# Kernel tuning notes

Measured on AMD Instinct MI355X. Metric: run time of the kernel, lower is better.

## Reference

```python
import jax, jax.numpy as jnp
import numpy as np

B, C_IN, C_OUT, H, K = 256, 64, 64, 1855, 6


def setup_inputs() -> dict:
    key = jax.random.key(0)
    k1, k2, k3, k4 = jax.random.split(key, 4)
    x = jax.random.normal(k1, (B, C_IN, H), dtype=jnp.float32)
    # hex-grid neighbor table; -1 marks missing neighbors (camera boundary).
    neighbors = jax.random.randint(k2, (H, K), 0, H, dtype=jnp.int32)
    # row 0 fully valid is not required -- module uses row 0 to compute total_valid.
    mask = jax.random.uniform(k3, (H, K)) < 0.1
    neighbors = jnp.where(mask, -1, neighbors)
    weight_center = jax.random.normal(k4, (C_OUT, C_IN), dtype=jnp.float32) / np.sqrt(C_IN)
    weight_neighbors = jax.random.normal(jax.random.fold_in(key, 5), (C_OUT, C_IN, K), dtype=jnp.float32) / np.sqrt(C_IN * K)
    bias = jnp.zeros((C_OUT,), dtype=jnp.float32)
    return {"x": x, "neighbors": neighbors, "weight_center": weight_center,
            "weight_neighbors": weight_neighbors, "bias": bias}


def reference(x, neighbors, weight_center, weight_neighbors, bias):
    # x: [B, C_in, H] -> [B, H, C_in]
    xt = jnp.swapaxes(x, 1, 2)
    # center contribution: [B, H, C_out]
    center = jnp.einsum('bhc,oc->bho', xt, weight_center)
    valid = neighbors >= 0                      # [H, K]
    idx = jnp.where(valid, neighbors, 0)        # safe gather indices
    nf = xt[:, idx]                             # [B, H, K, C_in] gathered neighbors
    nf = nf * valid[None, :, :, None].astype(xt.dtype)
    neighbor_contrib = jnp.einsum('bhkc,ock->bho', nf, weight_neighbors)
    # module divides by (#valid neighbors of hexagon 0) + 1
    total_valid = (valid[0].sum() + 1).astype(xt.dtype)
    out = (center + neighbor_contrib) / total_valid + bias
    return jnp.swapaxes(out, 1, 2)              # [B, C_out, H]
```

## Files before the change

### kernel.cpp

```cpp
#include <hip/hip_runtime.h>
#include <hip/hip_bf16.h>

#define B_    256
#define CIN   64
#define COUT  64
#define H_    1855
#define K_    6
#define KDIM  448
#define NSTEP 14
#define HT    64
#define NHT   29

#define HT2   32
#define TPB   58
#define NTILE (TPB * B_)
#define TPBLK 8
#define NBLK  (NTILE / TPBLK)
#define CPX2  (NBLK / 8)

typedef __bf16 bf16x8 __attribute__((ext_vector_type(8)));
typedef float  f32x4  __attribute__((ext_vector_type(4)));

typedef __attribute__((address_space(3))) unsigned int       lds_u32;
typedef const __attribute__((address_space(1))) unsigned int glb_u32;

static __device__ inline unsigned short f2bf(float f) {
    __hip_bfloat16 h = __float2bfloat16(f);
    return *reinterpret_cast<unsigned short*>(&h);
}

__global__ void prep_weights(const float* __restrict__ wc,
                             const float* __restrict__ wn,
                             const int*   __restrict__ nb,
                             unsigned short* __restrict__ W2,
                             float* __restrict__ inv_tv,
                             unsigned short* __restrict__ zbuf) {
    int e = blockIdx.x * 256 + threadIdx.x;
    int j = e & 7;
    int l = (e >> 3) & 63;
    int t = (e >> 9) & 3;
    int s = e >> 11;
    int o = t * 16 + (l & 15);
    int k = s * 32 + (l >> 4) * 8 + j;
    int slot = k >> 6;
    int c = k & 63;
    float v = (slot == 0) ? wc[o * 64 + c]
                          : wn[(o * 64 + c) * 6 + (slot - 1)];
    W2[e] = f2bf(v);
    if (blockIdx.x == 0 && threadIdx.x < 64) zbuf[threadIdx.x] = 0;
    if (e == 0) {
        int cnt = 1;
        #pragma unroll
        for (int q = 0; q < 6; ++q) cnt += (nb[q] >= 0) ? 1 : 0;
        *inv_tv = 1.0f / (float)cnt;
    }
}

__global__ void transpose_bf16(const float* __restrict__ x,
                               unsigned short* __restrict__ xT) {
    __shared__ __align__(16) unsigned short tile[64][72];
    int b  = blockIdx.y;
    int h0 = blockIdx.x * HT;
    int t  = threadIdx.x;
    int ho = t & 63;
    int cq = t >> 6;
    const float* xb = x + (size_t)b * CIN * H_;
    int h = h0 + ho;
    #pragma unroll
    for (int i = 0; i < 16; ++i) {
        int c = i * 4 + cq;
        float v = (h < H_) ? xb[(size_t)c * H_ + h] : 0.f;
        tile[ho][c] = f2bf(v);
    }
    __syncthreads();
    #pragma unroll
    for (int rep = 0; rep < 2; ++rep) {
        int task = rep * 256 + t;
        int hh = task >> 3;
        int j  = task & 7;
        int hw = h0 + hh;
        if (hw < H_) {
            *reinterpret_cast<uint4*>(&xT[((size_t)b * H_ + hw) * 64 + j * 8]) =
                *reinterpret_cast<const uint4*>(&tile[hh][j * 8]);
        }
    }
}

__global__ __launch_bounds__(512, 4) void conv_main(
        const unsigned short* __restrict__ xT,
        const unsigned short* __restrict__ W2,
        const int*   __restrict__ nb,
        const float* __restrict__ bias,
        const float* __restrict__ inv_tv,
        const unsigned short* __restrict__ zbuf,
        float* __restrict__ out) {
    __shared__ __align__(16) unsigned short feat[2][7][HT2][64];

    int bid = blockIdx.x;
    int swz   = (bid & 7) * CPX2 + (bid >> 3);
    int gbase = swz * TPBLK;

    int t = threadIdx.x;
    int w = t >> 6;
    int l = t & 63;

    int lrow = l >> 3;
    int jsrc = (l & 7) ^ lrow;
    int q    = w - 1;

    int og = w & 3, hh = w >> 2;
    int lr = l & 15, lg = l >> 4;
    int hrow = hh * 16 + lr;

    const bf16x8* __restrict__ Wf = reinterpret_cast<const bf16x8*>(W2);
    bf16x8 wr[NSTEP];
    #pragma unroll
    for (int s = 0; s < NSTEP; ++s) wr[s] = Wf[(s * 4 + og) * 64 + l];
    float inv = *inv_tv;
    float bv[4];
    #pragma unroll
    for (int r = 0; r < 4; ++r) bv[r] = bias[og * 16 + lg * 4 + r];

    int nbv[4];
    int bn, h0n;

    if (w < 7) {
        int b0  = gbase / TPB;
        int h00 = (gbase - b0 * TPB) * HT2;
        #pragma unroll
        for (int c = 0; c < 4; ++c) {
            int h = h00 + c * 8 + lrow;
            nbv[c] = (h < H_) ? ((w == 0) ? h : nb[h * 6 + q]) : -1;
        }
        const unsigned short* xb = xT + (size_t)b0 * H_ * 64;
        #pragma unroll
        for (int c = 0; c < 4; ++c) {
            int n = nbv[c];
            const unsigned short* src = (n >= 0)
                ? (xb + (size_t)n * 64 + jsrc * 8) : (zbuf + jsrc * 8);
            __builtin_amdgcn_global_load_lds((glb_u32*)src,
                (lds_u32*)&feat[0][w][c * 8][0], 16, 0, 0);
        }
        int g1 = gbase + 1;
        bn  = g1 / TPB;
        h0n = (g1 - bn * TPB) * HT2;
        #pragma unroll
        for (int c = 0; c < 4; ++c) {
            int h = h0n + c * 8 + lrow;
            nbv[c] = (h < H_) ? ((w == 0) ? h : nb[h * 6 + q]) : -1;
        }
    }

    #pragma unroll 2
    for (int i = 0; i < TPBLK; ++i) {
        if (i < TPBLK - 1 && w < 7) {
            const unsigned short* xb = xT + (size_t)bn * H_ * 64;
            #pragma unroll
            for (int c = 0; c < 4; ++c) {
                int n = nbv[c];
                const unsigned short* src = (n >= 0)
                    ? (xb + (size_t)n * 64 + jsrc * 8) : (zbuf + jsrc * 8);
                __builtin_amdgcn_global_load_lds((glb_u32*)src,
                    (lds_u32*)&feat[(i + 1) & 1][w][c * 8][0], 16, 0, 0);
            }
        }
        if (i < TPBLK - 2 && w < 7) {
            int g2 = gbase + i + 2;
            bn  = g2 / TPB;
            h0n = (g2 - bn * TPB) * HT2;
            #pragma unroll
            for (int c = 0; c < 4; ++c) {
                int h = h0n + c * 8 + lrow;
                nbv[c] = (h < H_) ? ((w == 0) ? h : nb[h * 6 + q]) : -1;
            }
        }
        if (w == 0 || i == TPBLK - 1)
            asm volatile("s_waitcnt vmcnt(4)" ::: "memory");
        else
            asm volatile("s_waitcnt vmcnt(8)" ::: "memory");
        __builtin_amdgcn_s_barrier();
        __builtin_amdgcn_sched_barrier(0);

        int cb = i & 1;
        f32x4 acc = (f32x4){0.f, 0.f, 0.f, 0.f};
        #pragma unroll
        for (int s = 0; s < NSTEP; ++s) {
            int c16 = (((s & 1) * 4 + lg)) ^ (hrow & 7);
            bf16x8 bfrag = *reinterpret_cast<const bf16x8*>(
                    &feat[cb][s >> 1][hrow][c16 * 8]);
            acc = __builtin_amdgcn_mfma_f32_16x16x32_bf16(wr[s], bfrag, acc, 0, 0, 0);
        }

        int g    = gbase + i;
        int curb = g / TPB;
        int curh = (g - curb * TPB) * HT2 + hrow;
        if (curh < H_) {
            float* ob = out + (size_t)curb * COUT * H_ + curh;
            #pragma unroll
            for (int r = 0; r < 4; ++r)
                ob[(size_t)(og * 16 + lg * 4 + r) * H_] = acc[r] * inv + bv[r];
        }

        __builtin_amdgcn_s_barrier();
    }
}

extern "C" void kernel_launch(void* const* d_in, const int* in_sizes, int n_in,
                              void* d_out, int out_size, void* d_ws, size_t ws_size,
                              hipStream_t stream) {
    const float* x    = (const float*)d_in[0];
    const int*   nb   = (const int*)  d_in[1];
    const float* wc   = (const float*)d_in[2];
    const float* wn   = (const float*)d_in[3];
    const float* bias = (const float*)d_in[4];
    float* out = (float*)d_out;

    char* ws = (char*)d_ws;
    unsigned short* W2     = (unsigned short*)ws;
    float*          inv_tv = (float*)(ws + 57344);
    unsigned short* zbuf   = (unsigned short*)(ws + 57472);
    unsigned short* xT     = (unsigned short*)(ws + 57600);

    prep_weights<<<112, 256, 0, stream>>>(wc, wn, nb, W2, inv_tv, zbuf);

    dim3 tgrid(NHT, B_);
    transpose_bf16<<<tgrid, 256, 0, stream>>>(x, xT);
    conv_main<<<NBLK, 512, 0, stream>>>(xT, W2, nb, bias, inv_tv, zbuf, out);
}
```

Baseline: 115.6 us.

## Halve conv block to 4 waves, each computing two output groups

Shrinks the conv block from 8 to 4 wavefronts. Each wave now computes two 16-wide output-channel groups from one shared B fragment, which reuses each LDS read across two MFMAs. The gather work is spread so each wave loads one or two neighbor slots, and the vmcnt waits are adjusted to match. This doubles the per-wave weight registers and gather load count and lowers the thread count per block, trading occupancy and latency hiding for fewer LDS reads.

```diff
diff --git a/kernel.cpp b/kernel.cpp
--- a/kernel.cpp
+++ b/kernel.cpp
@@ -86,7 +86,7 @@
     }
 }
 
-__global__ __launch_bounds__(512, 4) void conv_main(
+__global__ __launch_bounds__(256, 2) void conv_main(
         const unsigned short* __restrict__ xT,
         const unsigned short* __restrict__ W2,
         const int*   __restrict__ nb,
@@ -106,40 +106,61 @@
 
     int lrow = l >> 3;
     int jsrc = (l & 7) ^ lrow;
-    int q    = w - 1;
-
-    int og = w & 3, hh = w >> 2;
+    int slotA = w;
+    int slotB = w + 4;
+    bool hasB = (w < 3);
+    int qA = slotA - 1;
+    int qB = slotB - 1;
+
+    int ogp = w & 1, hh = w >> 1;
     int lr = l & 15, lg = l >> 4;
     int hrow = hh * 16 + lr;
 
     const bf16x8* __restrict__ Wf = reinterpret_cast<const bf16x8*>(W2);
-    bf16x8 wr[NSTEP];
-    #pragma unroll
-    for (int s = 0; s < NSTEP; ++s) wr[s] = Wf[(s * 4 + og) * 64 + l];
+    bf16x8 wr[NSTEP][2];
+    #pragma unroll
+    for (int s = 0; s < NSTEP; ++s)
+        #pragma unroll
+        for (int u = 0; u < 2; ++u)
+            wr[s][u] = Wf[(s * 4 + ogp * 2 + u) * 64 + l];
     float inv = *inv_tv;
-    float bv[4];
-    #pragma unroll
-    for (int r = 0; r < 4; ++r) bv[r] = bias[og * 16 + lg * 4 + r];
-
-    int nbv[4];
+    float bv0[4], bv1[4];
+    #pragma unroll
+    for (int r = 0; r < 4; ++r) {
+        bv0[r] = bias[ogp * 32 + lg * 4 + r];
+        bv1[r] = bias[ogp * 32 + 16 + lg * 4 + r];
+    }
+
+    int nbvA[4], nbvB[4];
     int bn, h0n;
 
-    if (w < 7) {
+    {
         int b0  = gbase / TPB;
         int h00 = (gbase - b0 * TPB) * HT2;
         #pragma unroll
         for (int c = 0; c < 4; ++c) {
             int h = h00 + c * 8 + lrow;
-            nbv[c] = (h < H_) ? ((w == 0) ? h : nb[h * 6 + q]) : -1;
+            nbvA[c] = (h < H_) ? ((qA < 0) ? h : nb[h * 6 + qA]) : -1;
+            nbvB[c] = (hasB && h < H_) ? nb[h * 6 + qB] : -1;
         }
         const unsigned short* xb = xT + (size_t)b0 * H_ * 64;
         #pragma unroll
         for (int c = 0; c < 4; ++c) {
-            int n = nbv[c];
+            int n = nbvA[c];
             const unsigned short* src = (n >= 0)
                 ? (xb + (size_t)n * 64 + jsrc * 8) : (zbuf + jsrc * 8);
             __builtin_amdgcn_global_load_lds((glb_u32*)src,
-                (lds_u32*)&feat[0][w][c * 8][0], 16, 0, 0);
+                (lds_u32*)&feat[0][slotA][c * 8][0], 16, 0, 0);
+        }
+        if (hasB) {
+            #pragma unroll
+            for (int c = 0; c < 4; ++c) {
+                int n = nbvB[c];
+                const unsigned short* src = (n >= 0)
+                    ? (xb + (size_t)n * 64 + jsrc * 8) : (zbuf + jsrc * 8);
+                __builtin_amdgcn_global_load_lds((glb_u32*)src,
+                    (lds_u32*)&feat[0][slotB][c * 8][0], 16, 0, 0);
+            }
         }
         int g1 = gbase + 1;
         bn  = g1 / TPB;
@@ -147,48 +168,63 @@
         #pragma unroll
         for (int c = 0; c < 4; ++c) {
             int h = h0n + c * 8 + lrow;
-            nbv[c] = (h < H_) ? ((w == 0) ? h : nb[h * 6 + q]) : -1;
+            nbvA[c] = (h < H_) ? ((qA < 0) ? h : nb[h * 6 + qA]) : -1;
+            nbvB[c] = (hasB && h < H_) ? nb[h * 6 + qB] : -1;
         }
     }
 
     #pragma unroll 2
     for (int i = 0; i < TPBLK; ++i) {
-        if (i < TPBLK - 1 && w < 7) {
+        if (i < TPBLK - 1) {
             const unsigned short* xb = xT + (size_t)bn * H_ * 64;
+            int nbuf = (i + 1) & 1;
             #pragma unroll
             for (int c = 0; c < 4; ++c) {
-                int n = nbv[c];
+                int n = nbvA[c];
                 const unsigned short* src = (n >= 0)
                     ? (xb + (size_t)n * 64 + jsrc * 8) : (zbuf + jsrc * 8);
                 __builtin_amdgcn_global_load_lds((glb_u32*)src,
-                    (lds_u32*)&feat[(i + 1) & 1][w][c * 8][0], 16, 0, 0);
-            }
-        }
-        if (i < TPBLK - 2 && w < 7) {
+                    (lds_u32*)&feat[nbuf][slotA][c * 8][0], 16, 0, 0);
+            }
+            if (hasB) {
+                #pragma unroll
+                for (int c = 0; c < 4; ++c) {
+                    int n = nbvB[c];
+                    const unsigned short* src = (n >= 0)
+                        ? (xb + (size_t)n * 64 + jsrc * 8) : (zbuf + jsrc * 8);
+                    __builtin_amdgcn_global_load_lds((glb_u32*)src,
+                        (lds_u32*)&feat[nbuf][slotB][c * 8][0], 16, 0, 0);
+                }
+            }
+        }
+        if (i < TPBLK - 2) {
             int g2 = gbase + i + 2;
             bn  = g2 / TPB;
             h0n = (g2 - bn * TPB) * HT2;
             #pragma unroll
             for (int c = 0; c < 4; ++c) {
                 int h = h0n + c * 8 + lrow;
-                nbv[c] = (h < H_) ? ((w == 0) ? h : nb[h * 6 + q]) : -1;
-            }
-        }
-        if (w == 0 || i == TPBLK - 1)
-            asm volatile("s_waitcnt vmcnt(4)" ::: "memory");
+                nbvA[c] = (h < H_) ? ((qA < 0) ? h : nb[h * 6 + qA]) : -1;
+                nbvB[c] = (hasB && h < H_) ? nb[h * 6 + qB] : -1;
+            }
+        }
+        if (w < 3 && i < TPBLK - 1)
+            asm volatile("s_waitcnt vmcnt(16)" ::: "memory");
         else
             asm volatile("s_waitcnt vmcnt(8)" ::: "memory");
         __builtin_amdgcn_s_barrier();
         __builtin_amdgcn_sched_barrier(0);
 
         int cb = i & 1;
-        f32x4 acc = (f32x4){0.f, 0.f, 0.f, 0.f};
+        f32x4 acc0 = (f32x4){0.f, 0.f, 0.f, 0.f};
+        f32x4 acc1 = (f32x4){0.f, 0.f, 0.f, 0.f};
         #pragma unroll
         for (int s = 0; s < NSTEP; ++s) {
             int c16 = (((s & 1) * 4 + lg)) ^ (hrow & 7);
             bf16x8 bfrag = *reinterpret_cast<const bf16x8*>(
                     &feat[cb][s >> 1][hrow][c16 * 8]);
-            acc = __builtin_amdgcn_mfma_f32_16x16x32_bf16(wr[s], bfrag, acc, 0, 0, 0);
+            acc0 = __builtin_amdgcn_mfma_f32_16x16x32_bf16(wr[s][0], bfrag, acc0, 0, 0, 0);
+            acc1 = __builtin_amdgcn_mfma_f32_16x16x32_bf16(wr[s][1], bfrag, acc1, 0, 0, 0);
         }
 
         int g    = gbase + i;
@@ -197,8 +233,10 @@
         if (curh < H_) {
             float* ob = out + (size_t)curb * COUT * H_ + curh;
             #pragma unroll
-            for (int r = 0; r < 4; ++r)
-                ob[(size_t)(og * 16 + lg * 4 + r) * H_] = acc[r] * inv + bv[r];
+            for (int r = 0; r < 4; ++r) {
+                ob[(size_t)(ogp * 32 + lg * 4 + r) * H_]      = acc0[r] * inv + bv0[r];
+                ob[(size_t)(ogp * 32 + 16 + lg * 4 + r) * H_] = acc1[r] * inv + bv1[r];
+            }
         }
 
         __builtin_amdgcn_s_barrier();
@@ -225,5 +263,5 @@
 
     dim3 tgrid(NHT, B_);
     transpose_bf16<<<tgrid, 256, 0, stream>>>(x, xT);
-    conv_main<<<NBLK, 512, 0, stream>>>(xT, W2, nb, bias, inv_tv, zbuf, out);
-}
+    conv_main<<<NBLK, 256, 0, stream>>>(xT, W2, nb, bias, inv_tv, zbuf, out);
+}
```

Result: slower. 119.6 us (+3.5%).

## Load center features directly into registers and spread neighbor gathers over all waves

Applied to the files above, without the earlier changes.

Center-pixel features are now loaded straight from global memory into registers (double-buffered) and fed to MFMA, no longer staged through LDS. The six neighbor slots' gather work is redistributed so all 8 waves issue 3 async global-to-LDS loads each, replacing 7 waves doing 4 each while one wave idled. LDS drops from 7 to 6 slots per buffer and the main loop is fully unrolled. Wait counts are retuned to the new load mix. This risks more register pressure and more VGPR-destination loads in flight.

```diff
diff --git a/kernel.cpp b/kernel.cpp
--- a/kernel.cpp
+++ b/kernel.cpp
@@ -6,7 +6,6 @@
 #define COUT  64
 #define H_    1855
 #define K_    6
-#define KDIM  448
 #define NSTEP 14
 #define HT    64
 #define NHT   29
@@ -94,7 +93,7 @@
         const float* __restrict__ inv_tv,
         const unsigned short* __restrict__ zbuf,
         float* __restrict__ out) {
-    __shared__ __align__(16) unsigned short feat[2][7][HT2][64];
+    __shared__ __align__(16) unsigned short feat[2][6][HT2][64];
 
     int bid = blockIdx.x;
     int swz   = (bid & 7) * CPX2 + (bid >> 3);
@@ -106,89 +105,115 @@
 
     int lrow = l >> 3;
     int jsrc = (l & 7) ^ lrow;
-    int q    = w - 1;
+    int qm[3], rq[3];
+    #pragma unroll
+    for (int c = 0; c < 3; ++c) {
+        int m = w * 3 + c;
+        qm[c] = m >> 2;
+        rq[c] = (m & 3) * 8;
+    }
 
     int og = w & 3, hh = w >> 2;
     int lr = l & 15, lg = l >> 4;
     int hrow = hh * 16 + lr;
+    int sw8  = hrow & 7;
 
     const bf16x8* __restrict__ Wf = reinterpret_cast<const bf16x8*>(W2);
     bf16x8 wr[NSTEP];
     #pragma unroll
     for (int s = 0; s < NSTEP; ++s) wr[s] = Wf[(s * 4 + og) * 64 + l];
+    #pragma unroll
+    for (int s = 0; s < NSTEP; ++s) asm volatile("" : "+v"(wr[s]));
+
     float inv = *inv_tv;
     float bv[4];
     #pragma unroll
     for (int r = 0; r < 4; ++r) bv[r] = bias[og * 16 + lg * 4 + r];
 
-    int nbv[4];
+    int nbv[3];
     int bn, h0n;
-
-    if (w < 7) {
+    bf16x8 cc[2][2];
+
+    {
         int b0  = gbase / TPB;
         int h00 = (gbase - b0 * TPB) * HT2;
         #pragma unroll
-        for (int c = 0; c < 4; ++c) {
-            int h = h00 + c * 8 + lrow;
-            nbv[c] = (h < H_) ? ((w == 0) ? h : nb[h * 6 + q]) : -1;
+        for (int c = 0; c < 3; ++c) {
+            int h = h00 + rq[c] + lrow;
+            nbv[c] = (h < H_) ? nb[h * 6 + qm[c]] : -1;
         }
         const unsigned short* xb = xT + (size_t)b0 * H_ * 64;
         #pragma unroll
-        for (int c = 0; c < 4; ++c) {
+        for (int c = 0; c < 3; ++c) {
             int n = nbv[c];
             const unsigned short* src = (n >= 0)
                 ? (xb + (size_t)n * 64 + jsrc * 8) : (zbuf + jsrc * 8);
             __builtin_amdgcn_global_load_lds((glb_u32*)src,
-                (lds_u32*)&feat[0][w][c * 8][0], 16, 0, 0);
-        }
+                (lds_u32*)&feat[0][qm[c]][rq[c]][0], 16, 0, 0);
+        }
+        int hcl = h00 + hrow; if (hcl >= H_) hcl = H_ - 1;
+        const bf16x8* crow = reinterpret_cast<const bf16x8*>(xb + (size_t)hcl * 64);
+        cc[0][0] = crow[lg];
+        cc[0][1] = crow[4 + lg];
         int g1 = gbase + 1;
         bn  = g1 / TPB;
         h0n = (g1 - bn * TPB) * HT2;
         #pragma unroll
-        for (int c = 0; c < 4; ++c) {
-            int h = h0n + c * 8 + lrow;
-            nbv[c] = (h < H_) ? ((w == 0) ? h : nb[h * 6 + q]) : -1;
-        }
-    }
-
-    #pragma unroll 2
+        for (int c = 0; c < 3; ++c) {
+            int h = h0n + rq[c] + lrow;
+            nbv[c] = (h < H_) ? nb[h * 6 + qm[c]] : -1;
+        }
+    }
+
+    #pragma unroll
     for (int i = 0; i < TPBLK; ++i) {
-        if (i < TPBLK - 1 && w < 7) {
+        if (i < TPBLK - 1) {
             const unsigned short* xb = xT + (size_t)bn * H_ * 64;
+            int nbuf = (i + 1) & 1;
             #pragma unroll
-            for (int c = 0; c < 4; ++c) {
+            for (int c = 0; c < 3; ++c) {
                 int n = nbv[c];
                 const unsigned short* src = (n >= 0)
                     ? (xb + (size_t)n * 64 + jsrc * 8) : (zbuf + jsrc * 8);
                 __builtin_amdgcn_global_load_lds((glb_u32*)src,
-                    (lds_u32*)&feat[(i + 1) & 1][w][c * 8][0], 16, 0, 0);
+                    (lds_u32*)&feat[nbuf][qm[c]][rq[c]][0], 16, 0, 0);
             }
-        }
-        if (i < TPBLK - 2 && w < 7) {
+            int hcl = h0n + hrow; if (hcl >= H_) hcl = H_ - 1;
+            const bf16x8* crow = reinterpret_cast<const bf16x8*>(xb + (size_t)hcl * 64);
+            cc[nbuf][0] = crow[lg];
+            cc[nbuf][1] = crow[4 + lg];
+        }
+        if (i < TPBLK - 2) {
             int g2 = gbase + i + 2;
             bn  = g2 / TPB;
             h0n = (g2 - bn * TPB) * HT2;
             #pragma unroll
-            for (int c = 0; c < 4; ++c) {
-                int h = h0n + c * 8 + lrow;
-                nbv[c] = (h < H_) ? ((w == 0) ? h : nb[h * 6 + q]) : -1;
+            for (int c = 0; c < 3; ++c) {
+                int h = h0n + rq[c] + lrow;
+                nbv[c] = (h < H_) ? nb[h * 6 + qm[c]] : -1;
             }
         }
-        if (w == 0 || i == TPBLK - 1)
-            asm volatile("s_waitcnt vmcnt(4)" ::: "memory");
+        if (i == TPBLK - 1)
+            asm volatile("s_waitcnt vmcnt(6)" ::: "memory");
+        else if (i == TPBLK - 2)
+            asm volatile("s_waitcnt vmcnt(9)" ::: "memory");
         else
-            asm volatile("s_waitcnt vmcnt(8)" ::: "memory");
+            asm volatile("s_waitcnt vmcnt(12)" ::: "memory");
         __builtin_amdgcn_s_barrier();
         __builtin_amdgcn_sched_barrier(0);
 
         int cb = i & 1;
         f32x4 acc = (f32x4){0.f, 0.f, 0.f, 0.f};
-        #pragma unroll
-        for (int s = 0; s < NSTEP; ++s) {
-            int c16 = (((s & 1) * 4 + lg)) ^ (hrow & 7);
-            bf16x8 bfrag = *reinterpret_cast<const bf16x8*>(
-                    &feat[cb][s >> 1][hrow][c16 * 8]);
-            acc = __builtin_amdgcn_mfma_f32_16x16x32_bf16(wr[s], bfrag, acc, 0, 0, 0);
+        acc = __builtin_amdgcn_mfma_f32_16x16x32_bf16(wr[0], cc[cb][0], acc, 0, 0, 0);
+        acc = __builtin_amdgcn_mfma_f32_16x16x32_bf16(wr[1], cc[cb][1], acc, 0, 0, 0);
+        #pragma unroll
+        for (int q = 0; q < 6; ++q) {
+            bf16x8 fa = *reinterpret_cast<const bf16x8*>(
+                    &feat[cb][q][hrow][(lg ^ sw8) * 8]);
+            bf16x8 fb = *reinterpret_cast<const bf16x8*>(
+                    &feat[cb][q][hrow][((4 + lg) ^ sw8) * 8]);
+            acc = __builtin_amdgcn_mfma_f32_16x16x32_bf16(wr[2 + 2 * q], fa, acc, 0, 0, 0);
+            acc = __builtin_amdgcn_mfma_f32_16x16x32_bf16(wr[3 + 2 * q], fb, acc, 0, 0, 0);
         }
 
         int g    = gbase + i;
```

Measured after the change: 129.7 us. 1.12x slower.

## Stage neighbor gathers through registers and use one barrier per tile iteration

Applied to the files above, without the earlier changes.

Replaces the direct global-to-LDS loads with ordinary 16-byte global loads into registers. The staged rows are written into the XOR-swizzled LDS buffer after the current tile's MFMA and output stores. The wait/barrier schedule is rearranged so each iteration needs a single lgkmcnt wait plus barrier, and the tile loop is fully unrolled. The aim is to cut synchronization stalls and give more control over load latency hiding, at the cost of extra VGPRs for the staging buffer and explicit LDS writes.

```diff
diff --git a/kernel.cpp b/kernel.cpp
--- a/kernel.cpp
+++ b/kernel.cpp
@@ -6,7 +6,6 @@
 #define COUT  64
 #define H_    1855
 #define K_    6
-#define KDIM  448
 #define NSTEP 14
 #define HT    64
 #define NHT   29
@@ -20,9 +19,6 @@
 
 typedef __bf16 bf16x8 __attribute__((ext_vector_type(8)));
 typedef float  f32x4  __attribute__((ext_vector_type(4)));
-
-typedef __attribute__((address_space(3))) unsigned int       lds_u32;
-typedef const __attribute__((address_space(1))) unsigned int glb_u32;
 
 static __device__ inline unsigned short f2bf(float f) {
     __hip_bfloat16 h = __float2bfloat16(f);
@@ -104,88 +100,92 @@
     int w = t >> 6;
     int l = t & 63;
 
-    int lrow = l >> 3;
-    int jsrc = (l & 7) ^ lrow;
-    int q    = w - 1;
+    int lrow   = l >> 3;
+    int lchunk = l & 7;
+    bool stg   = (w < 7);
+    int q      = w - 1;
 
     int og = w & 3, hh = w >> 2;
     int lr = l & 15, lg = l >> 4;
     int hrow = hh * 16 + lr;
+    int sw8  = hrow & 7;
 
     const bf16x8* __restrict__ Wf = reinterpret_cast<const bf16x8*>(W2);
     bf16x8 wr[NSTEP];
     #pragma unroll
     for (int s = 0; s < NSTEP; ++s) wr[s] = Wf[(s * 4 + og) * 64 + l];
+
     float inv = *inv_tv;
     float bv[4];
     #pragma unroll
     for (int r = 0; r < 4; ++r) bv[r] = bias[og * 16 + lg * 4 + r];
 
-    int nbv[4];
-    int bn, h0n;
-
-    if (w < 7) {
+    int   nbv[4];
+    uint4 vstg[4];
+
+    {
         int b0  = gbase / TPB;
         int h00 = (gbase - b0 * TPB) * HT2;
-        #pragma unroll
-        for (int c = 0; c < 4; ++c) {
-            int h = h00 + c * 8 + lrow;
-            nbv[c] = (h < H_) ? ((w == 0) ? h : nb[h * 6 + q]) : -1;
-        }
-        const unsigned short* xb = xT + (size_t)b0 * H_ * 64;
-        #pragma unroll
-        for (int c = 0; c < 4; ++c) {
-            int n = nbv[c];
-            const unsigned short* src = (n >= 0)
-                ? (xb + (size_t)n * 64 + jsrc * 8) : (zbuf + jsrc * 8);
-            __builtin_amdgcn_global_load_lds((glb_u32*)src,
-                (lds_u32*)&feat[0][w][c * 8][0], 16, 0, 0);
-        }
-        int g1 = gbase + 1;
-        bn  = g1 / TPB;
-        h0n = (g1 - bn * TPB) * HT2;
-        #pragma unroll
-        for (int c = 0; c < 4; ++c) {
-            int h = h0n + c * 8 + lrow;
-            nbv[c] = (h < H_) ? ((w == 0) ? h : nb[h * 6 + q]) : -1;
-        }
-    }
-
-    #pragma unroll 2
+        if (stg) {
+            #pragma unroll
+            for (int c = 0; c < 4; ++c) {
+                int h = h00 + c * 8 + lrow;
+                int n = (h < H_) ? ((q < 0) ? h : nb[h * 6 + q]) : -1;
+                const unsigned short* src = (n >= 0)
+                    ? (xT + ((size_t)b0 * H_ + n) * 64 + lchunk * 8)
+                    : (zbuf + lchunk * 8);
+                vstg[c] = *reinterpret_cast<const uint4*>(src);
+            }
+            int g1  = gbase + 1;
+            int b1  = g1 / TPB;
+            int h01 = (g1 - b1 * TPB) * HT2;
+            #pragma unroll
+            for (int c = 0; c < 4; ++c) {
+                int h = h01 + c * 8 + lrow;
+                nbv[c] = (h < H_) ? ((q < 0) ? h : nb[h * 6 + q]) : -1;
+            }
+            #pragma unroll
+            for (int c = 0; c < 4; ++c)
+                *reinterpret_cast<uint4*>(
+                    &feat[0][w][c * 8 + lrow][(lchunk ^ lrow) * 8]) = vstg[c];
+        }
+        asm volatile("s_waitcnt lgkmcnt(0)" ::: "memory");
+        __builtin_amdgcn_s_barrier();
+        __builtin_amdgcn_sched_barrier(0);
+    }
+
+    #pragma unroll
     for (int i = 0; i < TPBLK; ++i) {
-        if (i < TPBLK - 1 && w < 7) {
-            const unsigned short* xb = xT + (size_t)bn * H_ * 64;
+        if (i < TPBLK - 1 && stg) {
+            int b1 = (gbase + i + 1) / TPB;
+            const unsigned short* xb1 = xT + (size_t)b1 * H_ * 64;
             #pragma unroll
             for (int c = 0; c < 4; ++c) {
                 int n = nbv[c];
                 const unsigned short* src = (n >= 0)
-                    ? (xb + (size_t)n * 64 + jsrc * 8) : (zbuf + jsrc * 8);
-                __builtin_amdgcn_global_load_lds((glb_u32*)src,
-                    (lds_u32*)&feat[(i + 1) & 1][w][c * 8][0], 16, 0, 0);
-            }
-        }
-        if (i < TPBLK - 2 && w < 7) {
-            int g2 = gbase + i + 2;
-            bn  = g2 / TPB;
-            h0n = (g2 - bn * TPB) * HT2;
-            #pragma unroll
-            for (int c = 0; c < 4; ++c) {
-                int h = h0n + c * 8 + lrow;
-                nbv[c] = (h < H_) ? ((w == 0) ? h : nb[h * 6 + q]) : -1;
-            }
-        }
-        if (w == 0 || i == TPBLK - 1)
-            asm volatile("s_waitcnt vmcnt(4)" ::: "memory");
-        else
-            asm volatile("s_waitcnt vmcnt(8)" ::: "memory");
-        __builtin_amdgcn_s_barrier();
+                    ? (xb1 + (size_t)n * 64 + lchunk * 8)
+                    : (zbuf + lchunk * 8);
+                vstg[c] = *reinterpret_cast<const uint4*>(src);
+            }
+        }
         __builtin_amdgcn_sched_barrier(0);
+
+        if (i < TPBLK - 2 && stg) {
+            int g2  = gbase + i + 2;
+            int b2  = g2 / TPB;
+            int h02 = (g2 - b2 * TPB) * HT2;
+            #pragma unroll
+            for (int c = 0; c < 4; ++c) {
+                int h = h02 + c * 8 + lrow;
+                nbv[c] = (h < H_) ? ((q < 0) ? h : nb[h * 6 + q]) : -1;
+            }
+        }
 
         int cb = i & 1;
         f32x4 acc = (f32x4){0.f, 0.f, 0.f, 0.f};
         #pragma unroll
         for (int s = 0; s < NSTEP; ++s) {
-            int c16 = (((s & 1) * 4 + lg)) ^ (hrow & 7);
+            int c16 = (((s & 1) * 4 + lg)) ^ sw8;
             bf16x8 bfrag = *reinterpret_cast<const bf16x8*>(
                     &feat[cb][s >> 1][hrow][c16 * 8]);
             acc = __builtin_amdgcn_mfma_f32_16x16x32_bf16(wr[s], bfrag, acc, 0, 0, 0);
@@ -201,7 +201,25 @@
                 ob[(size_t)(og * 16 + lg * 4 + r) * H_] = acc[r] * inv + bv[r];
         }
 
-        __builtin_amdgcn_s_barrier();
+        if (i < TPBLK - 1 && stg) {
+            if (q >= 0 && i < TPBLK - 2)
+                asm volatile("s_waitcnt vmcnt(8)" ::: "memory");
+            else
+                asm volatile("s_waitcnt vmcnt(4)" ::: "memory");
+            __builtin_amdgcn_sched_barrier(0);
+            int nbuf = (i + 1) & 1;
+            #pragma unroll
+            for (int c = 0; c < 4; ++c)
+                *reinterpret_cast<uint4*>(
+                    &feat[nbuf][w][c * 8 + lrow][(lchunk ^ lrow) * 8]) = vstg[c];
+        }
+
+        if (i < TPBLK - 1) {
+            __builtin_amdgcn_sched_barrier(0);
+            asm volatile("s_waitcnt lgkmcnt(0)" ::: "memory");
+            __builtin_amdgcn_s_barrier();
+            __builtin_amdgcn_sched_barrier(0);
+        }
     }
 }
 
```

Result: slower. 215.4 us (+86.3%).
